# Optimization experiments

Hardware: AMD Instinct MI355X
Metric: run time of the kernel (lower is better)

Reference implementation:

```python
import jax, jax.numpy as jnp
import numpy as np

T, IN, H, OUT, L = 2048, 128, 128, 128, 2


def setup_inputs() -> dict:
    key = jax.random.key(0)
    ks = jax.random.split(key, 12)
    s_in = 1.0 / np.sqrt(IN)
    s_h = 1.0 / np.sqrt(H)
    s_ff = 1.0 / np.sqrt(2 * H)
    return {
        "emb": jax.random.normal(ks[0], (T, IN), jnp.float32),
        "start": jax.random.randint(ks[1], (T,), 0, 2).astype(jnp.int32),
        "w_in": jax.random.normal(ks[2], (H, IN), jnp.float32) * s_in,
        "b_in": jnp.zeros((H,), jnp.float32),
        "w_out": jax.random.normal(ks[3], (OUT, H), jnp.float32) * s_h,
        "b_out": jnp.zeros((OUT,), jnp.float32),
        "w_f": jax.random.normal(ks[4], (L, 1, H), jnp.float32) * s_h,
        "b_f": jnp.zeros((L, 1), jnp.float32),
        "w_i": jax.random.normal(ks[5], (L, 1, H), jnp.float32) * s_h,
        "b_i": jnp.zeros((L, 1), jnp.float32),
        "w_v": jax.random.normal(ks[6], (L, H, H), jnp.float32) * s_h,
        "b_v": jnp.zeros((L, H), jnp.float32),
        "w_q": jax.random.normal(ks[7], (L, H, H), jnp.float32) * s_h,
        "b_q": jnp.zeros((L, H), jnp.float32),
        "w_k": jax.random.normal(ks[8], (L, H, H), jnp.float32) * s_h,
        "b_k": jnp.zeros((L, H), jnp.float32),
        "w_o": jax.random.normal(ks[9], (L, H, H), jnp.float32) * s_h,
        "b_o": jnp.zeros((L, H), jnp.float32),
        "w_ff": jax.random.normal(ks[10], (L, H, 2 * H), jnp.float32) * s_ff,
        "b_ff": jnp.zeros((L, H), jnp.float32),
    }


def _mlstm_layer(x, gate_mask, w_f, b_f, w_i, b_i, w_v, b_v, w_q, b_q, w_k, b_k, w_o, b_o):
    # x: [T, H] layer input; gate_mask: [T] (0.0 at episode starts -> reset)
    Hdim = x.shape[-1]
    i = jnp.exp(x @ w_i.T + b_i)                           # [T, 1] exp input gate
    v = x @ w_v.T + b_v                                    # [T, H]
    k = (x * (1.0 / np.sqrt(Hdim))) @ w_k.T + b_k          # [T, H] (1/sqrt(H) applied before Linear)
    C = i[:, :, None] * (v[:, :, None] * k[:, None, :])    # [T, H, H] gated outer products
    n = i * k                                              # [T, H]
    g = jax.nn.sigmoid(x @ w_f.T + b_f)[:, 0] * gate_mask  # [T] forget gate, zeroed at resets

    def step(carry, inp):
        S, m = carry
        Ct, nt, gt = inp
        S = gt * S + Ct
        m = gt * m + nt
        return (S, m), (S, m)

    init = (jnp.zeros((Hdim, Hdim), x.dtype), jnp.zeros((Hdim,), x.dtype))
    _, (S_all, m_all) = jax.lax.scan(step, init, (C, n, g))  # [T,H,H], [T,H]

    q = x @ w_q.T + b_q                                    # [T, H]
    o = jax.nn.sigmoid(x @ w_o.T + b_o)                    # [T, H]
    num = jnp.einsum('thk,tk->th', S_all, q)               # C @ q per step
    den = jnp.maximum(jnp.abs(jnp.einsum('th,th->t', m_all, q))[:, None], 1.0)
    return o * (num / den)


def reference(emb, start, w_in, b_in, w_out, b_out, w_f, b_f, w_i, b_i,
              w_v, b_v, w_q, b_q, w_k, b_k, w_o, b_o, w_ff, b_ff):
    gate_mask = 1.0 - start.astype(emb.dtype)              # reset => discard previous state
    e = emb @ w_in.T + b_in                                # [T, H]
    z = e
    for l in range(w_f.shape[0]):
        h = _mlstm_layer(z, gate_mask, w_f[l], b_f[l], w_i[l], b_i[l],
                         w_v[l], b_v[l], w_q[l], b_q[l], w_k[l], b_k[l], w_o[l], b_o[l])
        z = jax.nn.leaky_relu(jnp.concatenate([h, e], axis=-1) @ w_ff[l].T + b_ff[l])
    return z @ w_out.T + b_out
```

## Files before the change

### kernel.cpp

```cpp
#include <hip/hip_runtime.h>
#include <math.h>

#define TT 2048
#define HH 128
#define ROWS 8
#define SP 132
#define XR 144
#define NBLK (TT / ROWS)

__device__ __forceinline__ float dot4(float4 a, float4 b) {
    return a.x * b.x + a.y * b.y + a.z * b.z + a.w * b.w;
}

__device__ __forceinline__ int xidx(int r, int k) {
    return r * XR + ((k >> 5) * 36) + (k & 31);
}

__device__ __forceinline__ float2 load_f2_agent(const float* p) {
    unsigned long long u = __hip_atomic_load((const unsigned long long*)p,
                                             __ATOMIC_RELAXED, __HIP_MEMORY_SCOPE_AGENT);
    float2 r;
    r.x = __uint_as_float((unsigned)(u & 0xffffffffull));
    r.y = __uint_as_float((unsigned)(u >> 32));
    return r;
}
__device__ __forceinline__ float load_f_agent(const float* p) {
    return __hip_atomic_load(p, __ATOMIC_RELAXED, __HIP_MEMORY_SCOPE_AGENT);
}
__device__ __forceinline__ void store_f_agent(float* p, float v) {
    __hip_atomic_store(p, v, __ATOMIC_RELAXED, __HIP_MEMORY_SCOPE_AGENT);
}

__global__ __launch_bounds__(256) void prep_kernel(
        const float* __restrict__ w_in, const float* __restrict__ w_out,
        const float* __restrict__ w_v, const float* __restrict__ w_q,
        const float* __restrict__ w_k, const float* __restrict__ w_o,
        const float* __restrict__ w_ff,
        float4* __restrict__ win_p, float4* __restrict__ wout_p,
        float4* __restrict__ wcat, float4* __restrict__ wff_p,
        unsigned* __restrict__ bar) {
    int i = blockIdx.x * 256 + threadIdx.x;
    if (blockIdx.x == 0 && threadIdx.x < 16) bar[threadIdx.x] = 0u;
    if (i < 4096) {
        int cg = i >> 7, col = i & 127;
        win_p[i] = ((const float4*)w_in)[col * 32 + cg];
    } else if (i < 8192) {
        int j = i - 4096, cg = j >> 7, col = j & 127;
        wout_p[j] = ((const float4*)w_out)[col * 32 + cg];
    } else if (i < 40960) {
        int j = i - 8192;
        int l = j >> 14, r = j & 16383, cg = r >> 9, col = r & 511;
        int sel = col >> 7, cm = col & 127;
        const float* s = (sel == 0 ? w_v : sel == 1 ? w_q : sel == 2 ? w_k : w_o) + l * HH * HH;
        wcat[j] = ((const float4*)s)[cm * 32 + cg];
    } else {
        int j = i - 40960;
        int l = j >> 13, r = j & 8191, cg = r >> 7, col = r & 127;
        const float* s = w_ff + l * HH * 256;
        wff_p[j] = ((const float4*)s)[col * 64 + cg];
    }
}

__device__ __forceinline__ void grid_barrier(unsigned* __restrict__ ctr) {
    __syncthreads();
    if (threadIdx.x == 0) {
        atomicAdd(ctr, 1u);
        while (__hip_atomic_load(ctr, __ATOMIC_RELAXED, __HIP_MEMORY_SCOPE_AGENT)
               < (unsigned)NBLK) {
            __builtin_amdgcn_s_sleep(8);
        }
    }
    __syncthreads();
}

__device__ __forceinline__ void attn_row(int t0,
        const float* __restrict__ kb, const float* __restrict__ vb,
        const float* __restrict__ qs, const float* __restrict__ os,
        const float* __restrict__ g, const float* __restrict__ iexp,
        float* __restrict__ hs) {
    int tid = threadIdx.x;
    int wv = tid >> 6, lane = tid & 63;
    int t = t0 + wv;
    float2 q2 = *(const float2*)(qs + wv * SP + 2 * lane);
    float2 o2 = *(const float2*)(os + wv * SP + 2 * lane);
    int tp = t;
    float2 k2 = load_f2_agent(kb + tp * HH + 2 * lane);
    float2 v2 = load_f2_agent(vb + tp * HH + 2 * lane);
    float ie = load_f_agent(iexp + tp), gv = load_f_agent(g + tp);
    float nx = 0.f, ny = 0.f, dsum = 0.f, decay = 1.f;
    while (true) {
        bool cont = (tp > 0) && (gv != 0.f);
        float2 k2n = {0.f, 0.f}, v2n = {0.f, 0.f};
        float ien = 0.f, gvn = 0.f;
        if (cont) {
            k2n = load_f2_agent(kb + (tp - 1) * HH + 2 * lane);
            v2n = load_f2_agent(vb + (tp - 1) * HH + 2 * lane);
            ien = load_f_agent(iexp + tp - 1); gvn = load_f_agent(g + tp - 1);
        }
        float p = k2.x * q2.x + k2.y * q2.y;
#pragma unroll
        for (int off = 1; off <= 32; off <<= 1) p += __shfl_xor(p, off, 64);
        float coeff = decay * ie * p;
        nx += coeff * v2.x; ny += coeff * v2.y; dsum += coeff;
        if (!cont) break;
        decay *= gv;
        tp--; k2 = k2n; v2 = v2n; ie = ien; gv = gvn;
    }
    float inv = 1.f / fmaxf(fabsf(dsum), 1.f);
    int d = 2 * lane;
    *(float2*)(hs + wv * XR + (d >> 5) * 36 + (d & 31)) =
        make_float2(o2.x * nx * inv, o2.y * ny * inv);
}

__device__ __forceinline__ void proj_fi(int t0, const float* __restrict__ xls,
        const float* __restrict__ w_f, const float* __restrict__ b_f,
        const float* __restrict__ w_i, const float* __restrict__ b_i,
        const int* __restrict__ start, float* __restrict__ g, float* __restrict__ iexp) {
    int tid = threadIdx.x;
    int wv = tid >> 6, lane = tid & 63;
    int d = 2 * lane;
    float2 xv = *(const float2*)(xls + wv * XR + (d >> 5) * 36 + (d & 31));
    float pf = xv.x * w_f[d] + xv.y * w_f[d + 1];
    float pi = xv.x * w_i[d] + xv.y * w_i[d + 1];
#pragma unroll
    for (int off = 1; off <= 32; off <<= 1) {
        pf += __shfl_xor(pf, off, 64);
        pi += __shfl_xor(pi, off, 64);
    }
    if (lane == 0) {
        int t = t0 + wv;
        store_f_agent(g + t, start[t] ? 0.f : 1.f / (1.f + expf(-(pf + b_f[0]))));
        store_f_agent(iexp + t, expf(pi + b_i[0]));
    }
}

__device__ __forceinline__ void proj_block(int t0, const float* __restrict__ xls,
        const float4* __restrict__ wc,
        const float* __restrict__ b_v, const float* __restrict__ b_q,
        const float* __restrict__ b_k, const float* __restrict__ b_o,
        float* __restrict__ kb, float* __restrict__ vb,
        float* __restrict__ qs, float* __restrict__ os) {
    int tid = threadIdx.x;
    int lane = tid & 63, wv = tid >> 6;
    int kc = lane >> 4, c = lane & 15;
    int rg = wv >> 2, cslot = (wv & 3) * 16 + c;
    float acc[4][4] = {};
    float acc2[4][4] = {};
#pragma unroll
    for (int j = 0; j < 8; ++j) {
        const float4* wb = wc + (kc * 8 + j) * 512;
        float4 w0 = wb[cslot];
        float4 w1 = wb[128 + cslot];
        float4 w2 = wb[256 + cslot];
        float4 w3 = wb[384 + cslot];
        float4 w0h = wb[64 + cslot];
        float4 w1h = wb[192 + cslot];
        float4 w2h = wb[320 + cslot];
        float4 w3h = wb[448 + cslot];
#pragma unroll
        for (int rr = 0; rr < 4; ++rr) {
            float4 x4 = *(const float4*)(xls + (rg * 4 + rr) * XR + kc * 36 + 4 * j);
            acc[0][rr] += dot4(x4, w0);
            acc[1][rr] += dot4(x4, w1);
            acc[2][rr] += dot4(x4, w2);
            acc[3][rr] += dot4(x4, w3);
            acc2[0][rr] += dot4(x4, w0h);
            acc2[1][rr] += dot4(x4, w1h);
            acc2[2][rr] += dot4(x4, w2h);
            acc2[3][rr] += dot4(x4, w3h);
        }
    }
#pragma unroll
    for (int m = 0; m < 4; ++m)
#pragma unroll
        for (int rr = 0; rr < 4; ++rr) {
            acc[m][rr] += __shfl_xor(acc[m][rr], 16, 64);
            acc[m][rr] += __shfl_xor(acc[m][rr], 32, 64);
            acc2[m][rr] += __shfl_xor(acc2[m][rr], 16, 64);
            acc2[m][rr] += __shfl_xor(acc2[m][rr], 32, 64);
        }
    if (kc == 0) {
        const float ks = 0.088388347648318447f;
#pragma unroll
        for (int h = 0; h < 2; ++h) {
            int col = cslot + 64 * h;
            float bv = b_v[col], bq = b_q[col], bk = b_k[col], bo = b_o[col];
#pragma unroll
            for (int rr = 0; rr < 4; ++rr) {
                int r = rg * 4 + rr, t = t0 + r;
                float av = (h == 0 ? acc[0][rr] : acc2[0][rr]);
                float aq = (h == 0 ? acc[1][rr] : acc2[1][rr]);
                float ak = (h == 0 ? acc[2][rr] : acc2[2][rr]);
                float ao = (h == 0 ? acc[3][rr] : acc2[3][rr]);
                store_f_agent(vb + t * HH + col, av + bv);
                qs[r * SP + col] = aq + bq;
                store_f_agent(kb + t * HH + col, ak * ks + bk);
                os[r * SP + col] = 1.f / (1.f + expf(-(ao + bo)));
            }
        }
    }
}

__device__ __forceinline__ void gemv128(int rg, int kc, int cslot,
        const float* __restrict__ xs, const float4* __restrict__ Wp, int k4base,
        float acc[2][4]) {
#pragma unroll
    for (int j = 0; j < 8; ++j) {
        int k4 = k4base + kc * 8 + j;
        float4 w0 = Wp[k4 * 128 + cslot];
        float4 w1 = Wp[k4 * 128 + 64 + cslot];
#pragma unroll
        for (int rr = 0; rr < 4; ++rr) {
            float4 x4 = *(const float4*)(xs + (rg * 4 + rr) * XR + kc * 36 + 4 * j);
            acc[0][rr] += dot4(x4, w0);
            acc[1][rr] += dot4(x4, w1);
        }
    }
}

__device__ __forceinline__ void ff_block(const float* __restrict__ hsb,
        const float* __restrict__ esb, const float4* __restrict__ wff,
        const float* __restrict__ b_ff, float* __restrict__ zs) {
    int tid = threadIdx.x;
    int lane = tid & 63, wv = tid >> 6;
    int kc = lane >> 4, c = lane & 15;
    int rg = wv >> 2, cslot = (wv & 3) * 16 + c;
    float acc[2][4] = {};
    gemv128(rg, kc, cslot, hsb, wff, 0, acc);
    gemv128(rg, kc, cslot, esb, wff, 32, acc);
#pragma unroll
    for (int h = 0; h < 2; ++h)
#pragma unroll
        for (int rr = 0; rr < 4; ++rr) {
            acc[h][rr] += __shfl_xor(acc[h][rr], 16, 64);
            acc[h][rr] += __shfl_xor(acc[h][rr], 32, 64);
        }
    if (kc == 0) {
#pragma unroll
        for (int h = 0; h < 2; ++h) {
            int col = cslot + 64 * h;
            float bb = b_ff[col];
#pragma unroll
            for (int rr = 0; rr < 4; ++rr) {
                int r = rg * 4 + rr;
                float a = acc[h][rr] + bb;
                a = a > 0.f ? a : 0.01f * a;
                zs[xidx(r, col)] = a;
            }
        }
    }
}

__device__ __forceinline__ void dense128(int t0, const float* __restrict__ xls,
        const float4* __restrict__ Wp, const float* __restrict__ b,
        float* __restrict__ yg, float* __restrict__ ys) {
    int tid = threadIdx.x;
    int lane = tid & 63, wv = tid >> 6;
    int kc = lane >> 4, c = lane & 15;
    int rg = wv >> 2, cslot = (wv & 3) * 16 + c;
    float acc[2][4] = {};
    gemv128(rg, kc, cslot, xls, Wp, 0, acc);
#pragma unroll
    for (int h = 0; h < 2; ++h)
#pragma unroll
        for (int rr = 0; rr < 4; ++rr) {
            acc[h][rr] += __shfl_xor(acc[h][rr], 16, 64);
            acc[h][rr] += __shfl_xor(acc[h][rr], 32, 64);
        }
    if (kc == 0) {
#pragma unroll
        for (int h = 0; h < 2; ++h) {
            int col = cslot + 64 * h;
            float bb = b[col];
#pragma unroll
            for (int rr = 0; rr < 4; ++rr) {
                int r = rg * 4 + rr;
                float a = acc[h][rr] + bb;
                if (ys) ys[xidx(r, col)] = a;
                if (yg) yg[(t0 + r) * HH + col] = a;
            }
        }
    }
}

__global__ __launch_bounds__(512, 2) void mega_kernel(
        const float* __restrict__ emb, const int* __restrict__ start,
        const float4* __restrict__ win_p, const float* __restrict__ b_in,
        const float4* __restrict__ wcat,
        const float* __restrict__ b_v, const float* __restrict__ b_q,
        const float* __restrict__ b_k, const float* __restrict__ b_o,
        const float* __restrict__ w_f, const float* __restrict__ b_f,
        const float* __restrict__ w_i, const float* __restrict__ b_i,
        const float4* __restrict__ wff_p, const float* __restrict__ b_ff,
        const float4* __restrict__ wout_p, const float* __restrict__ b_out,
        float* __restrict__ k0b, float* __restrict__ v0b,
        float* __restrict__ k1b, float* __restrict__ v1b,
        float* __restrict__ g0, float* __restrict__ i0,
        float* __restrict__ g1, float* __restrict__ i1,
        unsigned* __restrict__ bar,
        float* __restrict__ out) {
    __shared__ float xs[ROWS * XR];
    __shared__ float es[ROWS * XR];
    __shared__ float hs[ROWS * XR];
    __shared__ float zs[ROWS * XR];
    __shared__ float qs[ROWS * SP];
    __shared__ float os[ROWS * SP];
    int tid = threadIdx.x;
    int t0 = blockIdx.x * ROWS;
    int wv = tid >> 6, lane = tid & 63;
    int d = 2 * lane;

    float2 ev = *(const float2*)(emb + (t0 + wv) * HH + d);
    *(float2*)(xs + wv * XR + (d >> 5) * 36 + (d & 31)) = ev;
    __syncthreads();
    dense128(t0, xs, win_p, b_in, (float*)0, es);
    __syncthreads();
    proj_block(t0, es, wcat, b_v, b_q, b_k, b_o, k0b, v0b, qs, os);
    proj_fi(t0, es, w_f, b_f, w_i, b_i, start, g0, i0);
    grid_barrier(bar + 0);

    attn_row(t0, k0b, v0b, qs, os, g0, i0, hs);
    __syncthreads();
    ff_block(hs, es, wff_p, b_ff, zs);
    __syncthreads();
    proj_block(t0, zs, wcat + 16384, b_v + HH, b_q + HH, b_k + HH, b_o + HH,
               k1b, v1b, qs, os);
    proj_fi(t0, zs, w_f + HH, b_f + 1, w_i + HH, b_i + 1, start, g1, i1);
    grid_barrier(bar + 1);

    attn_row(t0, k1b, v1b, qs, os, g1, i1, hs);
    __syncthreads();
    ff_block(hs, es, wff_p + 8192, b_ff + HH, zs);
    __syncthreads();
    dense128(t0, zs, wout_p, b_out, out, (float*)0);
}

extern "C" void kernel_launch(void* const* d_in, const int* in_sizes, int n_in,
                              void* d_out, int out_size, void* d_ws, size_t ws_size,
                              hipStream_t stream) {
    const float* emb   = (const float*)d_in[0];
    const int*   start = (const int*)  d_in[1];
    const float* w_in  = (const float*)d_in[2];
    const float* b_in  = (const float*)d_in[3];
    const float* w_out = (const float*)d_in[4];
    const float* b_out = (const float*)d_in[5];
    const float* w_f   = (const float*)d_in[6];
    const float* b_f   = (const float*)d_in[7];
    const float* w_i   = (const float*)d_in[8];
    const float* b_i   = (const float*)d_in[9];
    const float* w_v   = (const float*)d_in[10];
    const float* b_v   = (const float*)d_in[11];
    const float* w_q   = (const float*)d_in[12];
    const float* b_q   = (const float*)d_in[13];
    const float* w_k   = (const float*)d_in[14];
    const float* b_k   = (const float*)d_in[15];
    const float* w_o   = (const float*)d_in[16];
    const float* b_o   = (const float*)d_in[17];
    const float* w_ff  = (const float*)d_in[18];
    const float* b_ff  = (const float*)d_in[19];
    float* out = (float*)d_out;

    unsigned* bar = (unsigned*)d_ws;
    float* ws = (float*)d_ws + 64;
    float* k0b = ws; ws += TT * HH;
    float* v0b = ws; ws += TT * HH;
    float* k1b = ws; ws += TT * HH;
    float* v1b = ws; ws += TT * HH;
    float* g0  = ws; ws += TT;
    float* i0  = ws; ws += TT;
    float* g1  = ws; ws += TT;
    float* i1  = ws; ws += TT;
    float4* win_p  = (float4*)ws; ws += 16384;
    float4* wout_p = (float4*)ws; ws += 16384;
    float4* wcat   = (float4*)ws; ws += 131072;
    float4* wff_p  = (float4*)ws; ws += 65536;

    prep_kernel<<<dim3(224), dim3(256), 0, stream>>>(
        w_in, w_out, w_v, w_q, w_k, w_o, w_ff, win_p, wout_p, wcat, wff_p, bar);
    mega_kernel<<<dim3(NBLK), dim3(512), 0, stream>>>(
        emb, start, win_p, b_in, wcat,
        b_v, b_q, b_k, b_o, w_f, b_f, w_i, b_i,
        wff_p, b_ff, wout_p, b_out,
        k0b, v0b, k1b, v1b, g0, i0, g1, i1,
        bar, out);
}
```

Measured before the change: 143.7 us.

## Stage FF weights into LDS asynchronously and remap GEMV thread layouts

```diff
diff --git a/kernel.cpp b/kernel.cpp
--- a/kernel.cpp
+++ b/kernel.cpp
@@ -73,6 +73,18 @@
     __syncthreads();
 }
 
+__device__ __forceinline__ void stage_wsh(const float4* __restrict__ src, float4* lds) {
+    int tid = threadIdx.x;
+    int wv = tid >> 6;
+#pragma unroll
+    for (int it = 0; it < 16; ++it) {
+        __builtin_amdgcn_global_load_lds(
+            (const __attribute__((address_space(1))) unsigned int*)(src + it * 512 + tid),
+            (__attribute__((address_space(3))) unsigned int*)(lds + it * 512 + wv * 64),
+            16, 0, 0);
+    }
+}
+
 __device__ __forceinline__ void attn_row(int t0,
         const float* __restrict__ kb, const float* __restrict__ vb,
         const float* __restrict__ qs, const float* __restrict__ os,
@@ -143,9 +155,8 @@
     int tid = threadIdx.x;
     int lane = tid & 63, wv = tid >> 6;
     int kc = lane >> 4, c = lane & 15;
-    int rg = wv >> 2, cslot = (wv & 3) * 16 + c;
-    float acc[4][4] = {};
-    float acc2[4][4] = {};
+    int cslot = wv * 16 + c;
+    float accv[8] = {}, accq[8] = {}, acck[8] = {}, acco[8] = {};
 #pragma unroll
     for (int j = 0; j < 8; ++j) {
         const float4* wb = wc + (kc * 8 + j) * 512;
@@ -153,100 +164,74 @@
         float4 w1 = wb[128 + cslot];
         float4 w2 = wb[256 + cslot];
         float4 w3 = wb[384 + cslot];
-        float4 w0h = wb[64 + cslot];
-        float4 w1h = wb[192 + cslot];
-        float4 w2h = wb[320 + cslot];
-        float4 w3h = wb[448 + cslot];
-#pragma unroll
-        for (int rr = 0; rr < 4; ++rr) {
-            float4 x4 = *(const float4*)(xls + (rg * 4 + rr) * XR + kc * 36 + 4 * j);
-            acc[0][rr] += dot4(x4, w0);
-            acc[1][rr] += dot4(x4, w1);
-            acc[2][rr] += dot4(x4, w2);
-            acc[3][rr] += dot4(x4, w3);
-            acc2[0][rr] += dot4(x4, w0h);
-            acc2[1][rr] += dot4(x4, w1h);
-            acc2[2][rr] += dot4(x4, w2h);
-            acc2[3][rr] += dot4(x4, w3h);
-        }
-    }
-#pragma unroll
-    for (int m = 0; m < 4; ++m)
-#pragma unroll
-        for (int rr = 0; rr < 4; ++rr) {
-            acc[m][rr] += __shfl_xor(acc[m][rr], 16, 64);
-            acc[m][rr] += __shfl_xor(acc[m][rr], 32, 64);
-            acc2[m][rr] += __shfl_xor(acc2[m][rr], 16, 64);
-            acc2[m][rr] += __shfl_xor(acc2[m][rr], 32, 64);
-        }
+#pragma unroll
+        for (int rr = 0; rr < 8; ++rr) {
+            float4 x4 = *(const float4*)(xls + rr * XR + kc * 36 + 4 * j);
+            accv[rr] += dot4(x4, w0);
+            accq[rr] += dot4(x4, w1);
+            acck[rr] += dot4(x4, w2);
+            acco[rr] += dot4(x4, w3);
+        }
+    }
+#pragma unroll
+    for (int rr = 0; rr < 8; ++rr) {
+        accv[rr] += __shfl_xor(accv[rr], 16, 64); accv[rr] += __shfl_xor(accv[rr], 32, 64);
+        accq[rr] += __shfl_xor(accq[rr], 16, 64); accq[rr] += __shfl_xor(accq[rr], 32, 64);
+        acck[rr] += __shfl_xor(acck[rr], 16, 64); acck[rr] += __shfl_xor(acck[rr], 32, 64);
+        acco[rr] += __shfl_xor(acco[rr], 16, 64); acco[rr] += __shfl_xor(acco[rr], 32, 64);
+    }
     if (kc == 0) {
         const float ks = 0.088388347648318447f;
-#pragma unroll
-        for (int h = 0; h < 2; ++h) {
-            int col = cslot + 64 * h;
-            float bv = b_v[col], bq = b_q[col], bk = b_k[col], bo = b_o[col];
-#pragma unroll
-            for (int rr = 0; rr < 4; ++rr) {
-                int r = rg * 4 + rr, t = t0 + r;
-                float av = (h == 0 ? acc[0][rr] : acc2[0][rr]);
-                float aq = (h == 0 ? acc[1][rr] : acc2[1][rr]);
-                float ak = (h == 0 ? acc[2][rr] : acc2[2][rr]);
-                float ao = (h == 0 ? acc[3][rr] : acc2[3][rr]);
-                store_f_agent(vb + t * HH + col, av + bv);
-                qs[r * SP + col] = aq + bq;
-                store_f_agent(kb + t * HH + col, ak * ks + bk);
-                os[r * SP + col] = 1.f / (1.f + expf(-(ao + bo)));
-            }
-        }
-    }
-}
-
-__device__ __forceinline__ void gemv128(int rg, int kc, int cslot,
-        const float* __restrict__ xs, const float4* __restrict__ Wp, int k4base,
-        float acc[2][4]) {
+        float bv = b_v[cslot], bq = b_q[cslot], bk = b_k[cslot], bo = b_o[cslot];
+#pragma unroll
+        for (int rr = 0; rr < 8; ++rr) {
+            int t = t0 + rr;
+            store_f_agent(vb + t * HH + cslot, accv[rr] + bv);
+            qs[rr * SP + cslot] = accq[rr] + bq;
+            store_f_agent(kb + t * HH + cslot, acck[rr] * ks + bk);
+            os[rr * SP + cslot] = 1.f / (1.f + expf(-(acco[rr] + bo)));
+        }
+    }
+}
+
+__device__ __forceinline__ void ff_block(const float* __restrict__ hsb,
+        const float* __restrict__ esb, const float4* wffl,
+        const float* __restrict__ b_ff, float* __restrict__ zs) {
+    int tid = threadIdx.x;
+    int lane = tid & 63, wv = tid >> 6;
+    int kc = lane >> 3, c = lane & 7;
+    int cslot = wv * 8 + c;
+    const float* xb = (kc < 4) ? hsb : esb;
+    int coff = (kc & 3) * 36;
+    float a0[8] = {}, a1[8] = {};
 #pragma unroll
     for (int j = 0; j < 8; ++j) {
-        int k4 = k4base + kc * 8 + j;
-        float4 w0 = Wp[k4 * 128 + cslot];
-        float4 w1 = Wp[k4 * 128 + 64 + cslot];
-#pragma unroll
-        for (int rr = 0; rr < 4; ++rr) {
-            float4 x4 = *(const float4*)(xs + (rg * 4 + rr) * XR + kc * 36 + 4 * j);
-            acc[0][rr] += dot4(x4, w0);
-            acc[1][rr] += dot4(x4, w1);
-        }
-    }
-}
-
-__device__ __forceinline__ void ff_block(const float* __restrict__ hsb,
-        const float* __restrict__ esb, const float4* __restrict__ wff,
-        const float* __restrict__ b_ff, float* __restrict__ zs) {
-    int tid = threadIdx.x;
-    int lane = tid & 63, wv = tid >> 6;
-    int kc = lane >> 4, c = lane & 15;
-    int rg = wv >> 2, cslot = (wv & 3) * 16 + c;
-    float acc[2][4] = {};
-    gemv128(rg, kc, cslot, hsb, wff, 0, acc);
-    gemv128(rg, kc, cslot, esb, wff, 32, acc);
-#pragma unroll
-    for (int h = 0; h < 2; ++h)
-#pragma unroll
-        for (int rr = 0; rr < 4; ++rr) {
-            acc[h][rr] += __shfl_xor(acc[h][rr], 16, 64);
-            acc[h][rr] += __shfl_xor(acc[h][rr], 32, 64);
-        }
+        const float4* wl = wffl + (kc * 8 + j) * 128;
+        float4 w0 = wl[cslot];
+        float4 w1 = wl[64 + cslot];
+#pragma unroll
+        for (int rr = 0; rr < 8; ++rr) {
+            float4 x4 = *(const float4*)(xb + rr * XR + coff + 4 * j);
+            a0[rr] += dot4(x4, w0);
+            a1[rr] += dot4(x4, w1);
+        }
+    }
+#pragma unroll
+    for (int rr = 0; rr < 8; ++rr) {
+        a0[rr] += __shfl_xor(a0[rr], 8, 64); a0[rr] += __shfl_xor(a0[rr], 16, 64);
+        a0[rr] += __shfl_xor(a0[rr], 32, 64);
+        a1[rr] += __shfl_xor(a1[rr], 8, 64); a1[rr] += __shfl_xor(a1[rr], 16, 64);
+        a1[rr] += __shfl_xor(a1[rr], 32, 64);
+    }
     if (kc == 0) {
-#pragma unroll
-        for (int h = 0; h < 2; ++h) {
-            int col = cslot + 64 * h;
-            float bb = b_ff[col];
-#pragma unroll
-            for (int rr = 0; rr < 4; ++rr) {
-                int r = rg * 4 + rr;
-                float a = acc[h][rr] + bb;
-                a = a > 0.f ? a : 0.01f * a;
-                zs[xidx(r, col)] = a;
-            }
+        float b0 = b_ff[cslot], b1 = b_ff[cslot + 64];
+#pragma unroll
+        for (int rr = 0; rr < 8; ++rr) {
+            float z0 = a0[rr] + b0, z1 = a1[rr] + b1;
+            z0 = z0 > 0.f ? z0 : 0.01f * z0;
+            z1 = z1 > 0.f ? z1 : 0.01f * z1;
+            zs[xidx(rr, cslot)] = z0;
+            zs[xidx(rr, cslot + 64)] = z1;
         }
     }
 }
@@ -256,28 +241,37 @@
         float* __restrict__ yg, float* __restrict__ ys) {
     int tid = threadIdx.x;
     int lane = tid & 63, wv = tid >> 6;
-    int kc = lane >> 4, c = lane & 15;
-    int rg = wv >> 2, cslot = (wv & 3) * 16 + c;
-    float acc[2][4] = {};
-    gemv128(rg, kc, cslot, xls, Wp, 0, acc);
-#pragma unroll
-    for (int h = 0; h < 2; ++h)
-#pragma unroll
-        for (int rr = 0; rr < 4; ++rr) {
-            acc[h][rr] += __shfl_xor(acc[h][rr], 16, 64);
-            acc[h][rr] += __shfl_xor(acc[h][rr], 32, 64);
-        }
+    int kc = lane >> 3, c = lane & 7;
+    int cslot = wv * 8 + c;
+    float a0[8] = {}, a1[8] = {};
+#pragma unroll
+    for (int j = 0; j < 4; ++j) {
+        float4 w0 = Wp[(kc * 4 + j) * 128 + cslot];
+        float4 w1 = Wp[(kc * 4 + j) * 128 + 64 + cslot];
+        int off = (kc >> 1) * 36 + (kc & 1) * 16 + 4 * j;
+#pragma unroll
+        for (int rr = 0; rr < 8; ++rr) {
+            float4 x4 = *(const float4*)(xls + rr * XR + off);
+            a0[rr] += dot4(x4, w0);
+            a1[rr] += dot4(x4, w1);
+        }
+    }
+#pragma unroll
+    for (int rr = 0; rr < 8; ++rr) {
+        a0[rr] += __shfl_xor(a0[rr], 8, 64); a0[rr] += __shfl_xor(a0[rr], 16, 64);
+        a0[rr] += __shfl_xor(a0[rr], 32, 64);
+        a1[rr] += __shfl_xor(a1[rr], 8, 64); a1[rr] += __shfl_xor(a1[rr], 16, 64);
+        a1[rr] += __shfl_xor(a1[rr], 32, 64);
+    }
     if (kc == 0) {
-#pragma unroll
-        for (int h = 0; h < 2; ++h) {
-            int col = cslot + 64 * h;
-            float bb = b[col];
-#pragma unroll
-            for (int rr = 0; rr < 4; ++rr) {
-                int r = rg * 4 + rr;
-                float a = acc[h][rr] + bb;
-                if (ys) ys[xidx(r, col)] = a;
-                if (yg) yg[(t0 + r) * HH + col] = a;
+        float b0 = b[cslot], b1 = b[cslot + 64];
+#pragma unroll
+        for (int rr = 0; rr < 8; ++rr) {
+            float y0 = a0[rr] + b0, y1 = a1[rr] + b1;
+            if (ys) { ys[xidx(rr, cslot)] = y0; ys[xidx(rr, cslot + 64)] = y1; }
+            if (yg) {
+                yg[(t0 + rr) * HH + cslot] = y0;
+                yg[(t0 + rr) * HH + cslot + 64] = y1;
             }
         }
     }
@@ -305,6 +299,7 @@
     __shared__ float zs[ROWS * XR];
     __shared__ float qs[ROWS * SP];
     __shared__ float os[ROWS * SP];
+    __shared__ float4 wsh[8192];
     int tid = threadIdx.x;
     int t0 = blockIdx.x * ROWS;
     int wv = tid >> 6, lane = tid & 63;
@@ -319,18 +314,20 @@
     proj_fi(t0, es, w_f, b_f, w_i, b_i, start, g0, i0);
     grid_barrier(bar + 0);
 
+    stage_wsh(wff_p, wsh);
     attn_row(t0, k0b, v0b, qs, os, g0, i0, hs);
     __syncthreads();
-    ff_block(hs, es, wff_p, b_ff, zs);
+    ff_block(hs, es, wsh, b_ff, zs);
     __syncthreads();
     proj_block(t0, zs, wcat + 16384, b_v + HH, b_q + HH, b_k + HH, b_o + HH,
                k1b, v1b, qs, os);
     proj_fi(t0, zs, w_f + HH, b_f + 1, w_i + HH, b_i + 1, start, g1, i1);
     grid_barrier(bar + 1);
 
+    stage_wsh(wff_p + 8192, wsh);
     attn_row(t0, k1b, v1b, qs, os, g1, i1, hs);
     __syncthreads();
-    ff_block(hs, es, wff_p + 8192, b_ff + HH, zs);
+    ff_block(hs, es, wsh, b_ff + HH, zs);
     __syncthreads();
     dense128(t0, zs, wout_p, b_out, out, (float*)0);
 }
```

Result: no change. 145.4 us (+1.2%).
